# Kernel optimization log

Measured on AMD Instinct MI355X. Metric: run time of the kernel, lower is better.

## Reference

```python
import jax, jax.numpy as jnp
import numpy as np

NUM_ITERS = 3
EPS = 1e-8
LN_EPS = 1e-5


def _ln(x, g, b):
    m = x.mean(-1, keepdims=True)
    v = ((x - m) ** 2).mean(-1, keepdims=True)
    return (x - m) * jax.lax.rsqrt(v + LN_EPS) * g + b


def setup_inputs() -> dict:
    key = jax.random.key(0)
    ks = jax.random.split(key, 20)
    B, S, N, C = 32, 16, 16384, 128
    H = C  # hidden_dim defaults to dim
    s = 0.02
    f32 = jnp.float32
    return {
        "slots": jax.random.normal(ks[0], (B, S, C), f32),
        "inputs": jax.random.normal(ks[1], (B, N, C), f32),
        # projections (stored [in,out]; y = x @ W)
        "Wq": jax.random.normal(ks[2], (C, C), f32) * s,
        "Wk": jax.random.normal(ks[3], (C, C), f32) * s,
        "Wv": jax.random.normal(ks[4], (C, C), f32) * s,
        # GRUCell params, gate order r,z,n (stored [in, 3C])
        "gru_wih": jax.random.normal(ks[5], (C, 3 * C), f32) * s,
        "gru_whh": jax.random.normal(ks[6], (C, 3 * C), f32) * s,
        "gru_bih": jnp.zeros((3 * C,), f32),
        "gru_bhh": jnp.zeros((3 * C,), f32),
        # MLP
        "mlp_w1": jax.random.normal(ks[7], (C, H), f32) * s,
        "mlp_b1": jnp.zeros((H,), f32),
        "mlp_w2": jax.random.normal(ks[8], (H, C), f32) * s,
        "mlp_b2": jnp.zeros((C,), f32),
        # LayerNorms
        "ln_in_g": jnp.ones((C,), f32),
        "ln_in_b": jnp.zeros((C,), f32),
        "ln_s_g": jnp.ones((C,), f32),
        "ln_s_b": jnp.zeros((C,), f32),
        "ln_ff_g": jnp.ones((C,), f32),
        "ln_ff_b": jnp.zeros((C,), f32),
    }


def reference(slots, inputs, Wq, Wk, Wv, gru_wih, gru_whh, gru_bih, gru_bhh,
              mlp_w1, mlp_b1, mlp_w2, mlp_b2,
              ln_in_g, ln_in_b, ln_s_g, ln_s_b, ln_ff_g, ln_ff_b):
    B, S, C = slots.shape
    scale = np.sqrt(C)
    x = _ln(inputs, ln_in_g, ln_in_b)          # pos_embed = Identity
    k = x @ Wk                                  # [B,N,C]
    v = x @ Wv                                  # [B,N,C]
    for _ in range(NUM_ITERS):
        slots_prev = slots
        q = (_ln(slots, ln_s_g, ln_s_b) @ Wq) / scale      # [B,S,C]
        dots = jnp.einsum('bqd,bkd->bqk', q, k)            # [B,S,N]
        attn = jax.nn.softmax(dots, axis=-2) + EPS         # softmax over slots
        attn = attn / attn.sum(-1, keepdims=True)          # renorm over keys
        updates = jnp.einsum('bkd,bqk->bqd', v, attn)      # [B,S,C]
        # GRUCell (torch semantics, gates r,z,n)
        gi = updates @ gru_wih + gru_bih
        gh = slots_prev @ gru_whh + gru_bhh
        ir, iz, in_ = jnp.split(gi, 3, axis=-1)
        hr, hz, hn = jnp.split(gh, 3, axis=-1)
        r = jax.nn.sigmoid(ir + hr)
        z = jax.nn.sigmoid(iz + hz)
        n = jnp.tanh(in_ + r * hn)
        slots = (1.0 - z) * n + z * slots_prev
        # residual MLP
        h = jax.nn.relu(_ln(slots, ln_ff_g, ln_ff_b) @ mlp_w1 + mlp_b1)
        slots = slots + (h @ mlp_w2 + mlp_b2)
    return slots
```

## Files before the change

### kernel.cpp

```cpp
#include <hip/hip_runtime.h>


#define NTOT 16384
#define CDIM 128

using short8 = __attribute__((ext_vector_type(8))) short;
using f32x4  = __attribute__((ext_vector_type(4))) float;
using u32x2  = __attribute__((ext_vector_type(2))) unsigned;

__device__ __forceinline__ unsigned pkbf(float lo, float hi) {
  unsigned r;
  asm("v_cvt_pk_bf16_f32 %0, %1, %2" : "=v"(r) : "v"(lo), "v"(hi));
  return r;
}
__device__ __forceinline__ float sigf(float x) { return 1.f / (1.f + __expf(-x)); }
__device__ __forceinline__ float tanhfast(float x) {
  x = fminf(fmaxf(x, -15.f), 15.f);
  float e = __expf(2.f * x);
  return (e - 1.f) / (e + 1.f);
}

__global__ __launch_bounds__(256) void k0_wqk(const float* __restrict__ Wq,
    const float* __restrict__ Wk, float* __restrict__ wqk) {
  int idx = blockIdx.x * 256 + threadIdx.x;
  int cq = idx >> 7, ck = idx & 127;
  const float* a = Wq + cq * 128;
  const float* b = Wk + ck * 128;
  float s = 0.f;
  #pragma unroll 8
  for (int i = 0; i < 128; i += 4) {
    f32x4 av = *(const f32x4*)(a + i), bv = *(const f32x4*)(b + i);
    s += av[0]*bv[0] + av[1]*bv[1] + av[2]*bv[2] + av[3]*bv[3];
  }
  wqk[idx] = s;
}

__global__ __launch_bounds__(256) void k1_ln(const float* __restrict__ in,
    const float* __restrict__ gam, const float* __restrict__ bet,
    unsigned short* __restrict__ xln) {
  __shared__ __align__(16) unsigned short xb[64 * 136];
  __shared__ float gs[128], bs[128];
  const int t = threadIdx.x, w = t >> 6, l = t & 63, lr = l & 15, lg = l >> 4;
  if (t < 128) { gs[t] = gam[t]; bs[t] = bet[t]; }
  const long rowbase = (long)blockIdx.x * 64;
  const float* src = in + (rowbase + w * 16 + lr) * CDIM;
  f32x4 x[4][2];
  #pragma unroll
  for (int kb = 0; kb < 4; ++kb) {
    x[kb][0] = *(const f32x4*)(src + kb * 32 + lg * 8);
    x[kb][1] = *(const f32x4*)(src + kb * 32 + lg * 8 + 4);
  }
  float s1 = 0.f, s2 = 0.f;
  #pragma unroll
  for (int kb = 0; kb < 4; ++kb)
    #pragma unroll
    for (int h = 0; h < 2; ++h)
      #pragma unroll
      for (int i = 0; i < 4; ++i) { float xx = x[kb][h][i]; s1 += xx; s2 += xx * xx; }
  s1 += __shfl_xor(s1, 16); s1 += __shfl_xor(s1, 32);
  s2 += __shfl_xor(s2, 16); s2 += __shfl_xor(s2, 32);
  const float mean = s1 * (1.f / 128.f);
  const float rstd = rsqrtf(s2 * (1.f / 128.f) - mean * mean + 1e-5f);
  __syncthreads();
  #pragma unroll
  for (int kb = 0; kb < 4; ++kb) {
    int c0 = kb * 32 + lg * 8;
    union { unsigned uw[4]; short8 s8; } cv;
    #pragma unroll
    for (int p = 0; p < 2; ++p) {
      float y0 = (x[kb][p][0] - mean) * rstd * gs[c0 + p*4 + 0] + bs[c0 + p*4 + 0];
      float y1 = (x[kb][p][1] - mean) * rstd * gs[c0 + p*4 + 1] + bs[c0 + p*4 + 1];
      float y2 = (x[kb][p][2] - mean) * rstd * gs[c0 + p*4 + 2] + bs[c0 + p*4 + 2];
      float y3 = (x[kb][p][3] - mean) * rstd * gs[c0 + p*4 + 3] + bs[c0 + p*4 + 3];
      cv.uw[p*2 + 0] = pkbf(y0, y1);
      cv.uw[p*2 + 1] = pkbf(y2, y3);
    }
    *(short8*)(xb + (w * 16 + lr) * 136 + c0) = cv.s8;
  }
  asm volatile("" ::: "memory");
  unsigned short* dst = xln + (rowbase + w * 16) * CDIM;
  #pragma unroll
  for (int i = 0; i < 4; ++i) {
    int row = i * 4 + (l >> 4), cb = (l & 15) * 8;
    short8 v = *(const short8*)(xb + (w * 16 + row) * 136 + cb);
    *(short8*)(dst + row * CDIM + cb) = v;
  }
}

__global__ __launch_bounds__(512) void kq_init(
    const float* __restrict__ slots, const float* __restrict__ lnsg,
    const float* __restrict__ lnsb, const float* __restrict__ wqk,
    unsigned short* __restrict__ qout) {
  const int b = blockIdx.x, t = threadIdx.x;
  const int s = t >> 5, jq = (t & 31) * 4;
  __shared__ __align__(16) float lnq[2048];
  f32x4 x4 = *(const f32x4*)(slots + b * 2048 + t * 4);
  float ps = x4[0] + x4[1] + x4[2] + x4[3];
  float pq = x4[0]*x4[0] + x4[1]*x4[1] + x4[2]*x4[2] + x4[3]*x4[3];
  ps += __shfl_xor(ps, 1); ps += __shfl_xor(ps, 2); ps += __shfl_xor(ps, 4); ps += __shfl_xor(ps, 8); ps += __shfl_xor(ps, 16);
  pq += __shfl_xor(pq, 1); pq += __shfl_xor(pq, 2); pq += __shfl_xor(pq, 4); pq += __shfl_xor(pq, 8); pq += __shfl_xor(pq, 16);
  float mean = ps * (1.f / 128.f);
  float var  = pq * (1.f / 128.f) - mean * mean;
  float rstd = rsqrtf(var + 1e-5f);
  f32x4 l4 = (x4 - mean) * rstd * (*(const f32x4*)(lnsg + jq)) + (*(const f32x4*)(lnsb + jq));
  *(f32x4*)(lnq + t * 4) = l4;
  __syncthreads();
  f32x4 qa = {0.f, 0.f, 0.f, 0.f};
  const float* wqp = wqk + jq;
  const float* qrow = lnq + s * 128;
  for (int c = 0; c < 128; ++c)
    qa += *(const f32x4*)(wqp + c * 128) * qrow[c];
  qa *= 0.08838834764831845f;
  u32x2 pk = { pkbf(qa[0], qa[1]), pkbf(qa[2], qa[3]) };
  *(u32x2*)(qout + b * 2048 + t * 4) = pk;
}

__global__ __launch_bounds__(256) void k2_attn(
    const unsigned short* __restrict__ xln, const unsigned short* __restrict__ qm,
    float* __restrict__ nump, float* __restrict__ denp) {
  const int nb = blockIdx.x, b = blockIdx.y;
  const int t = threadIdx.x, w = t >> 6, l = t & 63, lr = l & 15, lg = l >> 4;
  __shared__ __align__(16) char smem[38912];
  char* T = smem + w * 8192;
  unsigned short* pbw = (unsigned short*)(smem + 32768) + w * 640;

  const unsigned short* xb = xln + (long)b * (NTOT * CDIM);
  const unsigned short* qb = qm + b * 2048;

  short8 qf[4];
  #pragma unroll
  for (int kk = 0; kk < 4; ++kk)
    qf[kk] = *(const short8*)(qb + lr * CDIM + kk * 32 + lg * 8);

  f32x4 acc[8];
  #pragma unroll
  for (int i = 0; i < 8; ++i) acc[i] = (f32x4){0.f, 0.f, 0.f, 0.f};
  f32x4 dacc = {0.f, 0.f, 0.f, 0.f};

  short8 g[2][8];
  {
    const unsigned short* ts = xb + (long)(nb * 512 + w * 32) * 128 + l * 8;
    #pragma unroll
    for (int k = 0; k < 8; ++k) g[0][k] = *(const short8*)(ts + k * 512);
  }

  #pragma unroll
  for (int it = 0; it < 4; ++it) {
    const int cur = it & 1;
    #pragma unroll
    for (int k = 0; k < 8; ++k) {
      const unsigned nl = (unsigned)(k * 4 + lg);
      unsigned wr = nl * 256 + ((((unsigned)lr) ^ (nl & 15u)) << 4);
      *(short8*)(T + wr) = g[cur][k];
    }
    if (it < 3) {
      const unsigned short* ts = xb + (long)(nb * 512 + ((it + 1) * 4 + w) * 32) * 128 + l * 8;
      #pragma unroll
      for (int k = 0; k < 8; ++k) g[cur ^ 1][k] = *(const short8*)(ts + k * 512);
    }
    asm volatile("" ::: "memory");
    short8 xcur[8];
    #pragma unroll
    for (int h = 0; h < 2; ++h)
      #pragma unroll
      for (int kk = 0; kk < 4; ++kk) {
        unsigned rd = (unsigned)((h * 16 + lr) * 256) +
                      ((((unsigned)(kk * 4 + lg)) ^ (unsigned)lr) << 4);
        xcur[h * 4 + kk] = *(const short8*)(T + rd);
      }
    #pragma unroll
    for (int r = 0; r < 8; ++r) {
      const int h = r >> 2, kk = r & 3;
      const unsigned wb = (unsigned)(kk * 2048 + lg * 512 + (h * 16 + lr) * 2);
      #pragma unroll
      for (int e = 0; e < 8; ++e) {
        unsigned key = ((((unsigned)e >> 1) & 3u) ^ (unsigned)lg) << 4;
        unsigned off = (wb + e * 64) ^ key;
        *(unsigned short*)(T + off) = (unsigned short)xcur[r][e];
      }
    }
    #pragma unroll
    for (int h = 0; h < 2; ++h) {
      f32x4 d = {0.f, 0.f, 0.f, 0.f};
      #pragma unroll
      for (int kk = 0; kk < 4; ++kk)
        d = __builtin_amdgcn_mfma_f32_16x16x32_bf16(qf[kk], xcur[h*4+kk], d, 0, 0, 0);
      float e0 = __expf(d[0]), e1 = __expf(d[1]), e2 = __expf(d[2]), e3 = __expf(d[3]);
      float cs = e0 + e1 + e2 + e3;
      cs += __shfl_xor(cs, 16);
      cs += __shfl_xor(cs, 32);
      float inv = 1.f / cs;
      float p0 = e0 * inv + 1e-8f, p1 = e1 * inv + 1e-8f,
            p2 = e2 * inv + 1e-8f, p3 = e3 * inv + 1e-8f;
      dacc[0] += p0; dacc[1] += p1; dacc[2] += p2; dacc[3] += p3;
      unsigned w01 = pkbf(p0, p1), w23 = pkbf(p2, p3);
      const int nn = h * 16 + lr;
      pbw[(lg*4 + 0) * 40 + nn] = (unsigned short)w01;
      pbw[(lg*4 + 1) * 40 + nn] = (unsigned short)(w01 >> 16);
      pbw[(lg*4 + 2) * 40 + nn] = (unsigned short)w23;
      pbw[(lg*4 + 3) * 40 + nn] = (unsigned short)(w23 >> 16);
    }
    asm volatile("" ::: "memory");
    short8 pf = *(const short8*)(pbw + lr * 40 + lg * 8);
    #pragma unroll
    for (int ct = 0; ct < 8; ++ct) {
      unsigned key = (((((unsigned)lr >> 1) & 3u) ^
                      (((unsigned)(ct * 2) + ((unsigned)lr >> 3)) & 3u)) << 4);
      unsigned off = ((unsigned)((ct*16 + lr) * 64 + lg * 16)) ^ key;
      short8 af = *(const short8*)(T + off);
      acc[ct] = __builtin_amdgcn_mfma_f32_16x16x32_bf16(af, pf, acc[ct], 0, 0, 0);
    }
    asm volatile("" ::: "memory");
  }

  #pragma unroll
  for (int m = 1; m <= 8; m <<= 1) {
    dacc[0] += __shfl_xor(dacc[0], m); dacc[1] += __shfl_xor(dacc[1], m);
    dacc[2] += __shfl_xor(dacc[2], m); dacc[3] += __shfl_xor(dacc[3], m);
  }
  __syncthreads();
  if (w >= 2) {
    float* rb = (float*)(smem + (w - 2) * 8192);
    #pragma unroll
    for (int ct = 0; ct < 8; ++ct)
      *(f32x4*)(rb + lr * 128 + ct * 16 + lg * 4) = acc[ct];
    if (lr == 0) {
      float* db = (float*)(smem + 32768) + (w - 2) * 16;
      #pragma unroll
      for (int r = 0; r < 4; ++r) db[lg * 4 + r] = dacc[r];
    }
  }
  __syncthreads();
  if (w < 2) {
    const float* rb = (float*)(smem + w * 8192);
    float* outp = nump + (((long)b * 32 + nb) * 2 + w) * 2048;
    #pragma unroll
    for (int ct = 0; ct < 8; ++ct) {
      f32x4 other = *(const f32x4*)(rb + lr * 128 + ct * 16 + lg * 4);
      *(f32x4*)(outp + lr * 128 + ct * 16 + lg * 4) = acc[ct] + other;
    }
    if (lr == 0) {
      const float* db = (float*)(smem + 32768) + w * 16;
      #pragma unroll
      for (int r = 0; r < 4; ++r)
        denp[(((long)b * 32 + nb) * 2 + w) * 16 + lg * 4 + r] =
            dacc[r] + db[lg * 4 + r];
    }
  }
}

__global__ __launch_bounds__(128) void k3_update(
    const float* __restrict__ sprev, const float* __restrict__ nump,
    const float* __restrict__ denp, const float* __restrict__ Wv,
    const float* __restrict__ wih, const float* __restrict__ whh,
    const float* __restrict__ bih, const float* __restrict__ bhh,
    const float* __restrict__ w1, const float* __restrict__ b1,
    const float* __restrict__ w2, const float* __restrict__ b2,
    const float* __restrict__ lnfg, const float* __restrict__ lnfb,
    const float* __restrict__ lnsg, const float* __restrict__ lnsb,
    const float* __restrict__ wqk,
    float* __restrict__ sout, unsigned short* __restrict__ qout, const int doq) {
  const int g = blockIdx.x, b = blockIdx.y, t = threadIdx.x;
  const int sl = t >> 5, jq = (t & 31) * 4;
  const int s = g * 4 + sl;
  const long base = (long)b * 2048 + g * 512;
  __shared__ __align__(16) float sp[512];
  __shared__ __align__(16) float upd[512];
  __shared__ __align__(16) float upd2[512];
  __shared__ __align__(16) float lnb[512];
  __shared__ __align__(16) float denred[4];

  if (t < 64) {
    f32x4 dv = *(const f32x4*)(denp + ((long)b * 64 + t) * 16 + g * 4);
    #pragma unroll
    for (int m = 1; m <= 32; m <<= 1) {
      dv[0] += __shfl_xor(dv[0], m); dv[1] += __shfl_xor(dv[1], m);
      dv[2] += __shfl_xor(dv[2], m); dv[3] += __shfl_xor(dv[3], m);
    }
    if (t == 0) *(f32x4*)denred = dv;
  }

  f32x4 hp4 = *(const f32x4*)(sprev + base + t * 4);
  *(f32x4*)(sp + t * 4) = hp4;

  f32x4 ns = {0.f, 0.f, 0.f, 0.f};
  const float* np = nump + (long)b * 131072 + s * 128 + jq;
  #pragma unroll 4
  for (int p = 0; p < 64; ++p) ns += *(const f32x4*)(np + (long)p * 2048);
  __syncthreads();
  *(f32x4*)(upd + t * 4) = ns * (1.f / denred[sl]);
  __syncthreads();

  f32x4 ud = {0,0,0,0};
  const float* nxr = upd + sl * 128;
  for (int c = 0; c < 128; ++c)
    ud += *(const f32x4*)(Wv + c * 128 + jq) * nxr[c];
  *(f32x4*)(upd2 + t * 4) = ud;
  __syncthreads();

  f32x4 ir = {0,0,0,0}, iz = {0,0,0,0}, inn = {0,0,0,0};
  f32x4 hr = {0,0,0,0}, hz = {0,0,0,0}, hn = {0,0,0,0};
  const float* wih_p = wih + jq;
  const float* whh_p = whh + jq;
  const float* ur  = upd2 + sl * 128;
  const float* hrw = sp + sl * 128;
  for (int c = 0; c < 128; ++c) {
    float u = ur[c], h = hrw[c];
    ir  += *(const f32x4*)(wih_p + c * 384)       * u;
    iz  += *(const f32x4*)(wih_p + c * 384 + 128) * u;
    inn += *(const f32x4*)(wih_p + c * 384 + 256) * u;
    hr  += *(const f32x4*)(whh_p + c * 384)       * h;
    hz  += *(const f32x4*)(whh_p + c * 384 + 128) * h;
    hn  += *(const f32x4*)(whh_p + c * 384 + 256) * h;
  }
  ir  += *(const f32x4*)(bih + jq);
  iz  += *(const f32x4*)(bih + 128 + jq);
  inn += *(const f32x4*)(bih + 256 + jq);
  hr  += *(const f32x4*)(bhh + jq);
  hz  += *(const f32x4*)(bhh + 128 + jq);
  hn  += *(const f32x4*)(bhh + 256 + jq);
  f32x4 snew;
  #pragma unroll
  for (int i = 0; i < 4; ++i) {
    float r = sigf(ir[i] + hr[i]);
    float z = sigf(iz[i] + hz[i]);
    float n = tanhfast(inn[i] + r * hn[i]);
    snew[i] = (1.f - z) * n + z * hp4[i];
  }

  float ps = snew[0] + snew[1] + snew[2] + snew[3];
  float pq = snew[0]*snew[0] + snew[1]*snew[1] + snew[2]*snew[2] + snew[3]*snew[3];
  ps += __shfl_xor(ps, 1); ps += __shfl_xor(ps, 2); ps += __shfl_xor(ps, 4); ps += __shfl_xor(ps, 8); ps += __shfl_xor(ps, 16);
  pq += __shfl_xor(pq, 1); pq += __shfl_xor(pq, 2); pq += __shfl_xor(pq, 4); pq += __shfl_xor(pq, 8); pq += __shfl_xor(pq, 16);
  float mean = ps * (1.f / 128.f);
  float var  = pq * (1.f / 128.f) - mean * mean;
  float rstd = rsqrtf(var + 1e-5f);
  f32x4 lf = (snew - mean) * rstd * (*(const f32x4*)(lnfg + jq)) + (*(const f32x4*)(lnfb + jq));
  *(f32x4*)(lnb + t * 4) = lf;
  __syncthreads();

  f32x4 ha = {0,0,0,0};
  const float* w1p = w1 + jq;
  const float* lrow = lnb + sl * 128;
  for (int c = 0; c < 128; ++c)
    ha += *(const f32x4*)(w1p + c * 128) * lrow[c];
  ha += *(const f32x4*)(b1 + jq);
  #pragma unroll
  for (int i = 0; i < 4; ++i) ha[i] = fmaxf(ha[i], 0.f);
  *(f32x4*)(upd + t * 4) = ha;
  __syncthreads();

  f32x4 oa = {0,0,0,0};
  const float* w2p = w2 + jq;
  const float* hrow = upd + sl * 128;
  for (int c = 0; c < 128; ++c)
    oa += *(const f32x4*)(w2p + c * 128) * hrow[c];
  oa += *(const f32x4*)(b2 + jq);
  f32x4 sf = snew + oa;
  *(f32x4*)(sout + base + t * 4) = sf;

  if (doq) {
    float qs = sf[0] + sf[1] + sf[2] + sf[3];
    float qz = sf[0]*sf[0] + sf[1]*sf[1] + sf[2]*sf[2] + sf[3]*sf[3];
    qs += __shfl_xor(qs, 1); qs += __shfl_xor(qs, 2); qs += __shfl_xor(qs, 4); qs += __shfl_xor(qs, 8); qs += __shfl_xor(qs, 16);
    qz += __shfl_xor(qz, 1); qz += __shfl_xor(qz, 2); qz += __shfl_xor(qz, 4); qz += __shfl_xor(qz, 8); qz += __shfl_xor(qz, 16);
    float m2 = qs * (1.f / 128.f);
    float v2 = qz * (1.f / 128.f) - m2 * m2;
    float rs2 = rsqrtf(v2 + 1e-5f);
    f32x4 lq = (sf - m2) * rs2 * (*(const f32x4*)(lnsg + jq)) + (*(const f32x4*)(lnsb + jq));
    *(f32x4*)(sp + t * 4) = lq;
    __syncthreads();
    f32x4 qa = {0,0,0,0};
    const float* wqp = wqk + jq;
    const float* qrow = sp + sl * 128;
    for (int c = 0; c < 128; ++c)
      qa += *(const f32x4*)(wqp + c * 128) * qrow[c];
    qa *= 0.08838834764831845f;
    u32x2 pk = { pkbf(qa[0], qa[1]), pkbf(qa[2], qa[3]) };
    *(u32x2*)(qout + base + t * 4) = pk;
  }
}

extern "C" void kernel_launch(void* const* d_in, const int* in_sizes, int n_in,
                              void* d_out, int out_size, void* d_ws, size_t ws_size,
                              hipStream_t stream) {
  (void)in_sizes; (void)n_in; (void)out_size; (void)ws_size;
  const float* slots = (const float*)d_in[0];
  const float* inputs = (const float*)d_in[1];
  const float* Wq  = (const float*)d_in[2];
  const float* Wk  = (const float*)d_in[3];
  const float* Wv  = (const float*)d_in[4];
  const float* wih = (const float*)d_in[5];
  const float* whh = (const float*)d_in[6];
  const float* bih = (const float*)d_in[7];
  const float* bhh = (const float*)d_in[8];
  const float* w1  = (const float*)d_in[9];
  const float* b1  = (const float*)d_in[10];
  const float* w2  = (const float*)d_in[11];
  const float* b2  = (const float*)d_in[12];
  const float* lnig = (const float*)d_in[13];
  const float* lnib = (const float*)d_in[14];
  const float* lnsg = (const float*)d_in[15];
  const float* lnsb = (const float*)d_in[16];
  const float* lnfg = (const float*)d_in[17];
  const float* lnfb = (const float*)d_in[18];

  char* ws = (char*)d_ws;
  unsigned short* xln  = (unsigned short*)(ws);
  unsigned short* qbuf = (unsigned short*)(ws + 134217728L);
  float* wqk  = (float*)(ws + 134348800L);
  float* nump = (float*)(ws + 134414336L);
  float* denp = (float*)(ws + 151191552L);
  float* sbuf = (float*)(ws + 151322624L);

  k0_wqk<<<64, 256, 0, stream>>>(Wq, Wk, wqk);
  k1_ln<<<8192, 256, 0, stream>>>(inputs, lnig, lnib, xln);
  kq_init<<<32, 512, 0, stream>>>(slots, lnsg, lnsb, wqk, qbuf);
  for (int it = 0; it < 3; ++it) {
    k2_attn<<<dim3(32, 32), 256, 0, stream>>>(xln, qbuf, nump, denp);
    const float* sprev = (it == 0) ? slots : sbuf;
    float* sdst = (it == 2) ? (float*)d_out : sbuf;
    k3_update<<<dim3(4, 32), 128, 0, stream>>>(sprev, nump, denp, Wv,
                                      wih, whh, bih, bhh, w1, b1, w2, b2,
                                      lnfg, lnfb, lnsg, lnsb, wqk,
                                      sdst, qbuf, (it < 2) ? 1 : 0);
  }
}
```

Baseline: 346.8 us.

## Double attention grid, reduce partials in-block, split reduction into separate kernel

```diff
diff --git a/kernel.cpp b/kernel.cpp
--- a/kernel.cpp
+++ b/kernel.cpp
@@ -123,6 +123,7 @@
   __shared__ __align__(16) char smem[38912];
   char* T = smem + w * 8192;
   unsigned short* pbw = (unsigned short*)(smem + 32768) + w * 640;
+  float* denpark = (float*)(smem + 32768 + 5120);
 
   const unsigned short* xb = xln + (long)b * (NTOT * CDIM);
   const unsigned short* qb = qm + b * 2048;
@@ -139,24 +140,24 @@
 
   short8 g[2][8];
   {
-    const unsigned short* ts = xb + (long)(nb * 512 + w * 32) * 128 + l * 8;
+    const unsigned short* ts = xb + (long)(nb * 256 + w * 32) * 128 + l * 8;
     #pragma unroll
     for (int k = 0; k < 8; ++k) g[0][k] = *(const short8*)(ts + k * 512);
   }
 
   #pragma unroll
-  for (int it = 0; it < 4; ++it) {
-    const int cur = it & 1;
+  for (int it = 0; it < 2; ++it) {
+    const int n0 = nb * 256 + it * 128 + w * 32;
     #pragma unroll
     for (int k = 0; k < 8; ++k) {
       const unsigned nl = (unsigned)(k * 4 + lg);
       unsigned wr = nl * 256 + ((((unsigned)lr) ^ (nl & 15u)) << 4);
-      *(short8*)(T + wr) = g[cur][k];
-    }
-    if (it < 3) {
-      const unsigned short* ts = xb + (long)(nb * 512 + ((it + 1) * 4 + w) * 32) * 128 + l * 8;
-      #pragma unroll
-      for (int k = 0; k < 8; ++k) g[cur ^ 1][k] = *(const short8*)(ts + k * 512);
+      *(short8*)(T + wr) = g[it][k];
+    }
+    if (it == 0) {
+      const unsigned short* ts = xb + (long)(nb * 256 + 128 + w * 32) * 128 + l * 8;
+      #pragma unroll
+      for (int k = 0; k < 8; ++k) g[1][k] = *(const short8*)(ts + k * 512);
     }
     asm volatile("" ::: "memory");
     short8 xcur[8];
@@ -218,40 +219,60 @@
     dacc[0] += __shfl_xor(dacc[0], m); dacc[1] += __shfl_xor(dacc[1], m);
     dacc[2] += __shfl_xor(dacc[2], m); dacc[3] += __shfl_xor(dacc[3], m);
   }
-  __syncthreads();
-  if (w >= 2) {
-    float* rb = (float*)(smem + (w - 2) * 8192);
+  if (w > 0) {
+    float* rb = (float*)T;
     #pragma unroll
     for (int ct = 0; ct < 8; ++ct)
       *(f32x4*)(rb + lr * 128 + ct * 16 + lg * 4) = acc[ct];
     if (lr == 0) {
-      float* db = (float*)(smem + 32768) + (w - 2) * 16;
-      #pragma unroll
-      for (int r = 0; r < 4; ++r) db[lg * 4 + r] = dacc[r];
-    }
-  }
-  __syncthreads();
-  if (w < 2) {
-    const float* rb = (float*)(smem + w * 8192);
-    float* outp = nump + (((long)b * 32 + nb) * 2 + w) * 2048;
+      #pragma unroll
+      for (int r = 0; r < 4; ++r) denpark[(w - 1) * 16 + lg * 4 + r] = dacc[r];
+    }
+  }
+  __syncthreads();
+  if (w == 0) {
+    float* outp = nump + (((long)b * 64) + nb) * 2048;
     #pragma unroll
     for (int ct = 0; ct < 8; ++ct) {
-      f32x4 other = *(const f32x4*)(rb + lr * 128 + ct * 16 + lg * 4);
-      *(f32x4*)(outp + lr * 128 + ct * 16 + lg * 4) = acc[ct] + other;
+      f32x4 sum = acc[ct];
+      #pragma unroll
+      for (int ww = 1; ww < 4; ++ww)
+        sum += *(const f32x4*)((float*)(smem + ww * 8192) + lr * 128 + ct * 16 + lg * 4);
+      *(f32x4*)(outp + lr * 128 + ct * 16 + lg * 4) = sum;
     }
     if (lr == 0) {
-      const float* db = (float*)(smem + 32768) + w * 16;
-      #pragma unroll
-      for (int r = 0; r < 4; ++r)
-        denp[(((long)b * 32 + nb) * 2 + w) * 16 + lg * 4 + r] =
-            dacc[r] + db[lg * 4 + r];
-    }
-  }
+      #pragma unroll
+      for (int r = 0; r < 4; ++r) {
+        float dsum = dacc[r] + denpark[lg * 4 + r] + denpark[16 + lg * 4 + r] +
+                     denpark[32 + lg * 4 + r];
+        denp[(((long)b * 64) + nb) * 16 + lg * 4 + r] = dsum;
+      }
+    }
+  }
+}
+
+__global__ __launch_bounds__(128) void kr_reduce(const float* __restrict__ nump,
+    const float* __restrict__ denp, float* __restrict__ upd) {
+  const int bs = blockIdx.x;
+  const int b = bs >> 4, s = bs & 15, t = threadIdx.x;
+  __shared__ float dsh;
+  if (t < 64) {
+    float d = denp[((long)b * 64 + t) * 16 + s];
+    d += __shfl_xor(d, 1); d += __shfl_xor(d, 2); d += __shfl_xor(d, 4);
+    d += __shfl_xor(d, 8); d += __shfl_xor(d, 16); d += __shfl_xor(d, 32);
+    if (t == 0) dsh = d;
+  }
+  float ns = 0.f;
+  const float* np = nump + (long)b * 131072 + s * 128 + t;
+  #pragma unroll 4
+  for (int p = 0; p < 64; ++p) ns += np[(long)p * 2048];
+  __syncthreads();
+  upd[b * 2048 + s * 128 + t] = ns / dsh;
 }
 
 __global__ __launch_bounds__(128) void k3_update(
-    const float* __restrict__ sprev, const float* __restrict__ nump,
-    const float* __restrict__ denp, const float* __restrict__ Wv,
+    const float* __restrict__ sprev, const float* __restrict__ upd_g,
+    const float* __restrict__ Wv,
     const float* __restrict__ wih, const float* __restrict__ whh,
     const float* __restrict__ bih, const float* __restrict__ bhh,
     const float* __restrict__ w1, const float* __restrict__ b1,
@@ -262,33 +283,16 @@
     float* __restrict__ sout, unsigned short* __restrict__ qout, const int doq) {
   const int g = blockIdx.x, b = blockIdx.y, t = threadIdx.x;
   const int sl = t >> 5, jq = (t & 31) * 4;
-  const int s = g * 4 + sl;
   const long base = (long)b * 2048 + g * 512;
   __shared__ __align__(16) float sp[512];
   __shared__ __align__(16) float upd[512];
   __shared__ __align__(16) float upd2[512];
   __shared__ __align__(16) float lnb[512];
-  __shared__ __align__(16) float denred[4];
-
-  if (t < 64) {
-    f32x4 dv = *(const f32x4*)(denp + ((long)b * 64 + t) * 16 + g * 4);
-    #pragma unroll
-    for (int m = 1; m <= 32; m <<= 1) {
-      dv[0] += __shfl_xor(dv[0], m); dv[1] += __shfl_xor(dv[1], m);
-      dv[2] += __shfl_xor(dv[2], m); dv[3] += __shfl_xor(dv[3], m);
-    }
-    if (t == 0) *(f32x4*)denred = dv;
-  }
 
   f32x4 hp4 = *(const f32x4*)(sprev + base + t * 4);
   *(f32x4*)(sp + t * 4) = hp4;
-
-  f32x4 ns = {0.f, 0.f, 0.f, 0.f};
-  const float* np = nump + (long)b * 131072 + s * 128 + jq;
-  #pragma unroll 4
-  for (int p = 0; p < 64; ++p) ns += *(const f32x4*)(np + (long)p * 2048);
-  __syncthreads();
-  *(f32x4*)(upd + t * 4) = ns * (1.f / denred[sl]);
+  f32x4 u4 = *(const f32x4*)(upd_g + base + t * 4);
+  *(f32x4*)(upd + t * 4) = u4;
   __syncthreads();
 
   f32x4 ud = {0,0,0,0};
@@ -411,16 +415,18 @@
   float* wqk  = (float*)(ws + 134348800L);
   float* nump = (float*)(ws + 134414336L);
   float* denp = (float*)(ws + 151191552L);
-  float* sbuf = (float*)(ws + 151322624L);
+  float* updg = (float*)(ws + 151322624L);
+  float* sbuf = (float*)(ws + 151584768L);
 
   k0_wqk<<<64, 256, 0, stream>>>(Wq, Wk, wqk);
   k1_ln<<<8192, 256, 0, stream>>>(inputs, lnig, lnib, xln);
   kq_init<<<32, 512, 0, stream>>>(slots, lnsg, lnsb, wqk, qbuf);
   for (int it = 0; it < 3; ++it) {
-    k2_attn<<<dim3(32, 32), 256, 0, stream>>>(xln, qbuf, nump, denp);
+    k2_attn<<<dim3(64, 32), 256, 0, stream>>>(xln, qbuf, nump, denp);
+    kr_reduce<<<512, 128, 0, stream>>>(nump, denp, updg);
     const float* sprev = (it == 0) ? slots : sbuf;
     float* sdst = (it == 2) ? (float*)d_out : sbuf;
-    k3_update<<<dim3(4, 32), 128, 0, stream>>>(sprev, nump, denp, Wv,
+    k3_update<<<dim3(4, 32), 128, 0, stream>>>(sprev, updg, Wv,
                                       wih, whh, bih, bhh, w1, b1, w2, b2,
                                       lnfg, lnfb, lnsg, lnsb, wqk,
                                       sdst, qbuf, (it < 2) ? 1 : 0);
```

New measurement: 372.8 us. +7.5%, slower.
